# Kernel tuning notes

Measured on AMD Instinct MI355X. Metric: run time of the kernel, lower is better.

The kernel has to match this reference:

```python
import jax, jax.numpy as jnp
import numpy as np

D_MODEL = 1024
N_HEADS = 16
D_K = D_MODEL // N_HEADS


def setup_inputs() -> dict:
    key = jax.random.key(0)
    ks = jax.random.split(key, 11)
    B, S = 2, 2048
    scale = 0.02
    inp = {
        "q": jax.random.normal(ks[0], (B, S, D_MODEL), jnp.float32),
        "k": jax.random.normal(ks[1], (B, S, D_MODEL), jnp.float32),
        "v": jax.random.normal(ks[2], (B, S, D_MODEL), jnp.float32),
        "w_q": jax.random.normal(ks[3], (D_MODEL, D_MODEL), jnp.float32) * scale,
        "b_q": jnp.zeros((D_MODEL,), jnp.float32),
        "w_k": jax.random.normal(ks[4], (D_MODEL, D_MODEL), jnp.float32) * scale,
        "b_k": jnp.zeros((D_MODEL,), jnp.float32),
        "w_v": jax.random.normal(ks[5], (D_MODEL, D_MODEL), jnp.float32) * scale,
        "b_v": jnp.zeros((D_MODEL,), jnp.float32),
        "w_o": jax.random.normal(ks[6], (D_MODEL, D_MODEL), jnp.float32) * scale,
        "b_o": jnp.zeros((D_MODEL,), jnp.float32),
    }
    return inp


def reference(q, k, v, w_q, b_q, w_k, b_k, w_v, b_v, w_o, b_o):
    B, S, _ = q.shape
    # projections (torch Linear: x @ W.T + b); split into heads -> [B, H, S, d]
    def proj(x, w, b):
        return (x @ w.T + b).reshape(B, S, N_HEADS, D_K).transpose(0, 2, 1, 3)
    qh = proj(q, w_q, b_q)
    kh = proj(k, w_k, b_k)
    vh = proj(v, w_v, b_v)
    scores = jnp.einsum("bhqd,bhkd->bhqk", qh, kh) / jnp.sqrt(
        jnp.asarray(D_K, jnp.float32))
    attn = jax.nn.softmax(scores, axis=-1)  # dropout = identity (eval)
    out = jnp.einsum("bhqk,bhkd->bhqd", attn, vh)
    out = out.transpose(0, 2, 1, 3).reshape(B, S, D_MODEL)
    return out @ w_o.T + b_o
```

## Files before the change

### kernel.cpp

```cpp
#include <hip/hip_runtime.h>

typedef unsigned short u16;
typedef unsigned int u32;
typedef __attribute__((ext_vector_type(4))) unsigned short u16x4;
typedef __attribute__((ext_vector_type(8))) unsigned short u16x8;
typedef __attribute__((ext_vector_type(8))) __bf16 bf16x8;
typedef __attribute__((ext_vector_type(4))) float f32x4;
typedef __attribute__((ext_vector_type(16))) float f32x16;

#define SEQ 2048
#define DMODEL 1024
#define LDP 3072
#define MM (DMODEL * DMODEL)
#define SC 0.18033688f

__device__ __forceinline__ u16 f2bf(float f) {
  unsigned u = __builtin_bit_cast(unsigned, f);
  u = (u + 0x7fffu + ((u >> 16) & 1u)) >> 16;
  return (u16)u;
}

__device__ __forceinline__ u32 cvtpk(float lo, float hi) {
  u32 r;
  asm volatile("v_cvt_pk_bf16_f32 %0, %1, %2" : "=v"(r) : "v"(lo), "v"(hi));
  return r;
}

__device__ __forceinline__ float fexp2(float x) {
#if __has_builtin(__builtin_amdgcn_exp2f)
  return __builtin_amdgcn_exp2f(x);
#else
  return exp2f(x);
#endif
}

__device__ __forceinline__ bf16x8 ldbf8(const u16* p) {
  return __builtin_bit_cast(bf16x8, *(const u16x8*)p);
}
__device__ __forceinline__ bf16x8 ldbf8c(const char* p) {
  return __builtin_bit_cast(bf16x8, *(const u16x8*)p);
}

__device__ __forceinline__ f32x4 mfma16(bf16x8 a, bf16x8 b, f32x4 c) {
  return __builtin_amdgcn_mfma_f32_16x16x32_bf16(a, b, c, 0, 0, 0);
}
__device__ __forceinline__ f32x16 mfma32(bf16x8 a, bf16x8 b, f32x16 c) {
  return __builtin_amdgcn_mfma_f32_32x32x16_bf16(a, b, c, 0, 0, 0);
}

__device__ __forceinline__ void gl16(const void* g, void* l) {
  __builtin_amdgcn_global_load_lds(
      (__attribute__((address_space(1))) void*)(size_t)g,
      (__attribute__((address_space(3))) void*)l, 16, 0, 0);
}

__global__ void cast_all_k(const float* __restrict__ q, const float* __restrict__ k,
                           const float* __restrict__ v, const float* __restrict__ wq,
                           const float* __restrict__ wk, const float* __restrict__ wv,
                           const float* __restrict__ wo, u16* __restrict__ dq,
                           u16* __restrict__ dk, u16* __restrict__ dv,
                           u16* __restrict__ wqkv, u16* __restrict__ wob) {
  int b = blockIdx.x;
  const float* s;
  u16* d;
  if (b < 6144) {
    const int z = b >> 11;
    s = z == 0 ? q : z == 1 ? k : v;
    d = z == 0 ? dq : z == 1 ? dk : dv;
    b &= 2047;
  } else {
    const int z = (b - 6144) >> 9;
    s = z == 0 ? wq : z == 1 ? wk : z == 2 ? wv : wo;
    d = z < 3 ? wqkv + (size_t)z * MM : wob;
    b = (b - 6144) & 511;
  }
  const size_t i = ((size_t)b * blockDim.x + threadIdx.x) * 8;
  const float4 a = *(const float4*)(s + i);
  const float4 c = *(const float4*)(s + i + 4);
  u16x8 o;
  o[0] = f2bf(a.x); o[1] = f2bf(a.y); o[2] = f2bf(a.z); o[3] = f2bf(a.w);
  o[4] = f2bf(c.x); o[5] = f2bf(c.y); o[6] = f2bf(c.z); o[7] = f2bf(c.w);
  *(u16x8*)(d + i) = o;
}

template <int OMODE>
__device__ __forceinline__ void gemm_bt_body(const u16* __restrict__ A,
                                             const u16* __restrict__ Bw,
                                             const float* __restrict__ bias,
                                             void* __restrict__ Cv, const int K,
                                             const int ldc, const int ncol0,
                                             const int m0, const int n0,
                                             const float osc) {
  __shared__ u16 As[128 * 32];
  __shared__ u16 Bs[128 * 32];
  const int tid = threadIdx.x;
  const int lane = tid & 63;
  const int w = tid >> 6;
  const int l15 = lane & 15;
  const int lg = lane >> 4;

  f32x4 acc[4][4] = {};

  const int arow = (w >> 1) * 64 + l15;
  const int brow = (w & 1) * 64 + l15;
  const int kfb = lg * 16;

  const int strow = w * 32 + (lane >> 2);
  const u16* Ag = A + (size_t)(m0 + strow) * K + (lane & 3) * 8;
  const u16* Bg = Bw + (size_t)(n0 + strow) * K + (lane & 3) * 8;
  const size_t rstep = (size_t)16 * K;
  char* AsL0 = (char*)As + w * 32 * 64;
  char* AsL1 = AsL0 + 16 * 64;
  char* BsL0 = (char*)Bs + w * 32 * 64;
  char* BsL1 = BsL0 + 16 * 64;

  for (int k0 = 0; k0 < K; k0 += 32) {
    __syncthreads();
    gl16(Ag + k0, AsL0);
    gl16(Ag + k0 + rstep, AsL1);
    gl16(Bg + k0, BsL0);
    gl16(Bg + k0 + rstep, BsL1);
    __syncthreads();
    bf16x8 af[4], bfv[4];
#pragma unroll
    for (int t = 0; t < 4; ++t) {
      af[t] = ldbf8c((char*)As + (arow + t * 16) * 64 + kfb);
      bfv[t] = ldbf8c((char*)Bs + (brow + t * 16) * 64 + kfb);
    }
    __builtin_amdgcn_s_setprio(1);
#pragma unroll
    for (int i = 0; i < 4; ++i)
#pragma unroll
      for (int j = 0; j < 4; ++j) acc[i][j] = mfma16(af[i], bfv[j], acc[i][j]);
    __builtin_amdgcn_s_setprio(0);
  }

  const int mrow = (w >> 1) * 64 + lg * 4;
  const int ncol = (w & 1) * 64 + l15;
#pragma unroll
  for (int j = 0; j < 4; ++j) {
    const int gn = n0 + ncol + j * 16;
    const float bia = bias[gn];
#pragma unroll
    for (int i = 0; i < 4; ++i) {
      const int gmb = m0 + mrow + i * 16;
#pragma unroll
      for (int r = 0; r < 4; ++r) {
        const float val = (acc[i][j][r] + bia) * osc;
        const int gm = gmb + r;
        if (OMODE == 0) {
          ((float*)Cv)[(size_t)gm * ldc + gn] = val;
        } else if (OMODE == 1) {
          ((u16*)Cv)[(size_t)gm * ldc + ncol0 + gn] = f2bf(val);
        } else {
          const int bb = gm >> 11, ss = gm & 2047;
          const int hh = gn >> 6, dd = gn & 63;
          ((u16*)Cv)[(((size_t)(bb * 16 + hh) * 64 + dd) << 11) + ss] = f2bf(val);
        }
      }
    }
  }
}

__global__ __launch_bounds__(256, 3) void gemm_qkv_k(
    const u16* __restrict__ qb, const u16* __restrict__ kb,
    const u16* __restrict__ vb, const u16* __restrict__ wqkv,
    const float* __restrict__ bq, const float* __restrict__ bk,
    const float* __restrict__ bv, u16* __restrict__ proj, u16* __restrict__ vtb) {
  const int b = blockIdx.x;
  const int xcd = b & 7;
  const int i = b >> 3;
  const int z = i >> 5;
  const int j = i & 31;
  const int m0 = (xcd * 4 + (j >> 3)) * 128;
  const int n0 = (j & 7) * 128;
  if (z == 2)
    gemm_bt_body<2>(vb, wqkv + 2 * (size_t)MM, bv, vtb, DMODEL, 0, 0, m0, n0,
                    1.0f);
  else
    gemm_bt_body<1>(z == 0 ? qb : kb, wqkv + (size_t)z * MM, z == 0 ? bq : bk,
                    proj, DMODEL, LDP, z * DMODEL, m0, n0, z == 0 ? SC : 1.0f);
}

__global__ __launch_bounds__(256, 3) void gemm_o_k(const u16* __restrict__ attnb,
                                                   const u16* __restrict__ wob,
                                                   const float* __restrict__ bo,
                                                   float* __restrict__ out) {
  const int b = blockIdx.x;
  const int xcd = b & 7;
  const int i = b >> 3;
  const int m0 = (xcd * 4 + (i >> 3)) * 128;
  const int n0 = (i & 7) * 128;
  gemm_bt_body<0>(attnb, wob, bo, out, DMODEL, DMODEL, 0, m0, n0, 1.0f);
}

__global__ __launch_bounds__(512, 2) void attn_k(const u16* __restrict__ proj,
                                                 const u16* __restrict__ vtb,
                                                 u16* __restrict__ outa) {
  __shared__ __align__(16) char smem[65536];
  const int b = blockIdx.x;
  const int slot = b >> 3;
  const int bh = (b & 7) * 4 + (slot >> 3);
  const int qB = (slot & 7) * 256;
  const int tid = threadIdx.x;
  const int lane = tid & 63;
  const int w = tid >> 6;
  const int g = w >> 2;
  const int wg = w & 3;
  const int tg = tid & 255;
  const size_t rb = (size_t)(bh >> 4) * SEQ;
  const int h = bh & 15;
  const int l31 = lane & 31;
  const int hi = lane >> 5;
  const int swzk = (l31 & 7) << 4;
  const int swzv = (l31 & 15) << 3;

  char* const ksb = smem + g * 32768;
  char* const vsb = ksb + 16384;

  const int qW = qB + wg * 64;
  const u16* qpA = proj + (rb + qW + l31) * LDP + h * 64 + hi * 8;
  const u16* qpB = qpA + (size_t)32 * LDP;
  bf16x8 qfA[4], qfB[4];
#pragma unroll
  for (int km = 0; km < 4; ++km) {
    qfA[km] = ldbf8(qpA + km * 16);
    qfB[km] = ldbf8(qpB + km * 16);
  }

  const int srow = tg >> 2;
  const int scol = (tg & 3) * 32;
  const int scel = scol >> 1;
  const int kz0 = srow * 128 + (scol ^ ((srow & 7) << 4));
  const int kz1 = srow * 128 + ((scol + 16) ^ ((srow & 7) << 4));
  const int vz0 = srow * 128 + (scol ^ ((srow & 15) << 3));
  const int vz1 = srow * 128 + ((scol + 8) ^ ((srow & 15) << 3));
  const int vz2 = srow * 128 + ((scol + 16) ^ ((srow & 15) << 3));
  const int vz3 = srow * 128 + ((scol + 24) ^ ((srow & 15) << 3));
  const u16* kg = proj + rb * LDP + DMODEL + h * 64;
  const u16* vg = vtb + (size_t)bh * 64 * SEQ;
  const int kvbase = g * (SEQ / 2);

  u16x8 ka0, ka1, va0, va1;
  {
    const u16* kr = kg + (size_t)(kvbase + srow) * LDP + scel;
    ka0 = *(const u16x8*)kr;
    ka1 = *(const u16x8*)(kr + 8);
    const u16* vr = vg + (size_t)srow * SEQ + kvbase + scel;
    va0 = *(const u16x8*)vr;
    va1 = *(const u16x8*)(vr + 8);
  }

  f32x16 oaA0 = {}, oaA1 = {}, oaB0 = {}, oaB1 = {};
  float lrunA = 0.f, lrunB = 0.f;
  int p = 0;

  for (int it = 0; it < SEQ / 128; ++it) {
    {
      char* kd = ksb + p * 8192;
      char* vd = vsb + p * 8192;
      *(u16x8*)(kd + kz0) = ka0;
      *(u16x8*)(kd + kz1) = ka1;
      *(u16x4*)(vd + vz0) = *(u16x4*)&va0;
      *(u16x4*)(vd + vz1) = *((u16x4*)&va0 + 1);
      *(u16x4*)(vd + vz2) = *(u16x4*)&va1;
      *(u16x4*)(vd + vz3) = *((u16x4*)&va1 + 1);
    }
    __syncthreads();
    if (it + 1 < SEQ / 128) {
      const int kvn = kvbase + (it + 1) * 64;
      const u16* kr = kg + (size_t)(kvn + srow) * LDP + scel;
      ka0 = *(const u16x8*)kr;
      ka1 = *(const u16x8*)(kr + 8);
      const u16* vr = vg + (size_t)srow * SEQ + kvn + scel;
      va0 = *(const u16x8*)vr;
      va1 = *(const u16x8*)(vr + 8);
    }
    const char* kp = ksb + p * 8192;
    const char* vp = vsb + p * 8192;
    f32x16 sA0 = {}, sA1 = {}, sB0 = {}, sB1 = {};
    __builtin_amdgcn_s_setprio(1);
#pragma unroll
    for (int km = 0; km < 4; ++km) {
      const int co = (km * 32 + hi * 16) ^ swzk;
      const bf16x8 k0 = ldbf8c(kp + l31 * 128 + co);
      const bf16x8 k1 = ldbf8c(kp + (32 + l31) * 128 + co);
      sA0 = mfma32(k0, qfA[km], sA0);
      sB0 = mfma32(k0, qfB[km], sB0);
      sA1 = mfma32(k1, qfA[km], sA1);
      sB1 = mfma32(k1, qfB[km], sB1);
    }
    __builtin_amdgcn_s_setprio(0);

#pragma unroll
    for (int r = 0; r < 16; ++r) sA0[r] = fexp2(sA0[r]);
#pragma unroll
    for (int r = 0; r < 16; ++r) sA1[r] = fexp2(sA1[r]);
#pragma unroll
    for (int r = 0; r < 16; ++r) sB0[r] = fexp2(sB0[r]);
#pragma unroll
    for (int r = 0; r < 16; ++r) sB1[r] = fexp2(sB1[r]);
#define SUM16(V)                                                        \
    ((((V[0] + V[1]) + (V[2] + V[3])) + ((V[4] + V[5]) + (V[6] + V[7]))) + \
     (((V[8] + V[9]) + (V[10] + V[11])) + ((V[12] + V[13]) + (V[14] + V[15]))))
    float rsA = SUM16(sA0) + SUM16(sA1);
    float rsB = SUM16(sB0) + SUM16(sB1);
#undef SUM16
    rsA += __shfl_xor(rsA, 32);
    rsB += __shfl_xor(rsB, 32);
    lrunA += rsA;
    lrunB += rsB;

    __builtin_amdgcn_s_setprio(1);
#define PCHUNK2(SA, SB, G, CB)                                           \
    {                                                                    \
      u16x8 pbuA, pbuB;                                                  \
      ((u32*)&pbuA)[0] = cvtpk(SA[G + 0], SA[G + 1]);                    \
      ((u32*)&pbuA)[1] = cvtpk(SA[G + 2], SA[G + 3]);                    \
      ((u32*)&pbuA)[2] = cvtpk(SA[G + 4], SA[G + 5]);                    \
      ((u32*)&pbuA)[3] = cvtpk(SA[G + 6], SA[G + 7]);                    \
      ((u32*)&pbuB)[0] = cvtpk(SB[G + 0], SB[G + 1]);                    \
      ((u32*)&pbuB)[1] = cvtpk(SB[G + 2], SB[G + 3]);                    \
      ((u32*)&pbuB)[2] = cvtpk(SB[G + 4], SB[G + 5]);                    \
      ((u32*)&pbuB)[3] = cvtpk(SB[G + 6], SB[G + 7]);                    \
      const bf16x8 pbA = __builtin_bit_cast(bf16x8, pbuA);               \
      const bf16x8 pbB = __builtin_bit_cast(bf16x8, pbuB);               \
      const int vc0 = ((CB) + 8 * hi) ^ swzv;                            \
      const int vc1 = ((CB) + 16 + 8 * hi) ^ swzv;                       \
      const char* vr0 = vp + l31 * 128;                                  \
      const char* vr1 = vp + (32 + l31) * 128;                           \
      u16x8 vf0, vf1;                                                    \
      *(u16x4*)&vf0       = *(const u16x4*)(vr0 + vc0);                  \
      *((u16x4*)&vf0 + 1) = *(const u16x4*)(vr0 + vc1);                  \
      *(u16x4*)&vf1       = *(const u16x4*)(vr1 + vc0);                  \
      *((u16x4*)&vf1 + 1) = *(const u16x4*)(vr1 + vc1);                  \
      const bf16x8 v0 = __builtin_bit_cast(bf16x8, vf0);                 \
      const bf16x8 v1 = __builtin_bit_cast(bf16x8, vf1);                 \
      oaA0 = mfma32(v0, pbA, oaA0);                                      \
      oaB0 = mfma32(v0, pbB, oaB0);                                      \
      oaA1 = mfma32(v1, pbA, oaA1);                                      \
      oaB1 = mfma32(v1, pbB, oaB1);                                      \
    }
    PCHUNK2(sA0, sB0, 0, 0)
    PCHUNK2(sA0, sB0, 8, 32)
    PCHUNK2(sA1, sB1, 0, 64)
    PCHUNK2(sA1, sB1, 8, 96)
#undef PCHUNK2
    __builtin_amdgcn_s_setprio(0);
    p ^= 1;
  }

  float* sc = (float*)smem;
  const int col = wg * 64 + lane;
  __syncthreads();
  if (g == 1) {
#pragma unroll
    for (int r = 0; r < 16; ++r) sc[r * 256 + col] = oaA0[r];
#pragma unroll
    for (int r = 0; r < 16; ++r) sc[(16 + r) * 256 + col] = oaA1[r];
    sc[32 * 256 + col] = lrunA;
  }
  __syncthreads();
  if (g == 0) {
#pragma unroll
    for (int r = 0; r < 16; ++r) oaA0[r] += sc[r * 256 + col];
#pragma unroll
    for (int r = 0; r < 16; ++r) oaA1[r] += sc[(16 + r) * 256 + col];
    lrunA += sc[32 * 256 + col];
  }
  __syncthreads();
  if (g == 1) {
#pragma unroll
    for (int r = 0; r < 16; ++r) sc[r * 256 + col] = oaB0[r];
#pragma unroll
    for (int r = 0; r < 16; ++r) sc[(16 + r) * 256 + col] = oaB1[r];
    sc[32 * 256 + col] = lrunB;
  }
  __syncthreads();
  if (g == 0) {
#pragma unroll
    for (int r = 0; r < 16; ++r) oaB0[r] += sc[r * 256 + col];
#pragma unroll
    for (int r = 0; r < 16; ++r) oaB1[r] += sc[(16 + r) * 256 + col];
    lrunB += sc[32 * 256 + col];

    const float invA = 1.0f / lrunA;
    u16* orowA = outa + (rb + qW + l31) * DMODEL + h * 64 + hi * 4;
#pragma unroll
    for (int gg = 0; gg < 4; ++gg) {
      u16x4 st0, st1;
      ((u32*)&st0)[0] = cvtpk(oaA0[4 * gg + 0] * invA, oaA0[4 * gg + 1] * invA);
      ((u32*)&st0)[1] = cvtpk(oaA0[4 * gg + 2] * invA, oaA0[4 * gg + 3] * invA);
      *(u16x4*)(orowA + 8 * gg) = st0;
      ((u32*)&st1)[0] = cvtpk(oaA1[4 * gg + 0] * invA, oaA1[4 * gg + 1] * invA);
      ((u32*)&st1)[1] = cvtpk(oaA1[4 * gg + 2] * invA, oaA1[4 * gg + 3] * invA);
      *(u16x4*)(orowA + 32 + 8 * gg) = st1;
    }
    const float invB = 1.0f / lrunB;
    u16* orowB = orowA + (size_t)32 * DMODEL;
#pragma unroll
    for (int gg = 0; gg < 4; ++gg) {
      u16x4 st0, st1;
      ((u32*)&st0)[0] = cvtpk(oaB0[4 * gg + 0] * invB, oaB0[4 * gg + 1] * invB);
      ((u32*)&st0)[1] = cvtpk(oaB0[4 * gg + 2] * invB, oaB0[4 * gg + 3] * invB);
      *(u16x4*)(orowB + 8 * gg) = st0;
      ((u32*)&st1)[0] = cvtpk(oaB1[4 * gg + 0] * invB, oaB1[4 * gg + 1] * invB);
      ((u32*)&st1)[1] = cvtpk(oaB1[4 * gg + 2] * invB, oaB1[4 * gg + 3] * invB);
      *(u16x4*)(orowB + 32 + 8 * gg) = st1;
    }
  }
}

extern "C" void kernel_launch(void* const* d_in, const int* in_sizes, int n_in,
                              void* d_out, int out_size, void* d_ws, size_t ws_size,
                              hipStream_t stream) {
  const float* q  = (const float*)d_in[0];
  const float* k  = (const float*)d_in[1];
  const float* v  = (const float*)d_in[2];
  const float* wq = (const float*)d_in[3];
  const float* bq = (const float*)d_in[4];
  const float* wk = (const float*)d_in[5];
  const float* bk = (const float*)d_in[6];
  const float* wv = (const float*)d_in[7];
  const float* bv = (const float*)d_in[8];
  const float* wo = (const float*)d_in[9];
  const float* bo = (const float*)d_in[10];

  const size_t NTOK = (size_t)2 * SEQ;
  const size_t NELE = NTOK * DMODEL;
  u16* qb    = (u16*)d_ws;
  u16* kb    = qb + NELE;
  u16* vb    = kb + NELE;
  u16* wqkv  = vb + NELE;
  u16* wob   = wqkv + 3 * (size_t)MM;
  u16* projb = wob + (size_t)MM;
  u16* vtb   = projb + NTOK * LDP;
  u16* attnb = qb;

  cast_all_k<<<8192, 256, 0, stream>>>(q, k, v, wq, wk, wv, wo, qb, kb, vb,
                                       wqkv, wob);
  gemm_qkv_k<<<768, 256, 0, stream>>>(qb, kb, vb, wqkv, bq, bk, bv, projb, vtb);
  attn_k<<<256, 512, 0, stream>>>(projb, vtb, attnb);
  gemm_o_k<<<256, 256, 0, stream>>>(attnb, wob, bo, (float*)d_out);
}
```

Baseline: 118.1 us.

## Stage K/V tiles via direct global-to-LDS loads with permuted V layout

Replaces the register-staged K/V loads (global to registers, then swizzled LDS stores) with direct global-to-LDS 16-byte loads (gl16) into a double buffer, issued one iteration ahead. To make this work, the V projection epilogue writes V^T with a permuted sequence index, so the V tile in LDS can be read with single 16-byte ldbf8c reads instead of paired 8-byte reads. This removes the VGPR round trip and the LDS store instructions, and it moves the barrier to the end of each iteration. The cost is a dependence on the producer-side permutation and a changed synchronisation pattern that must still order the async LDS writes correctly.

```diff
diff --git a/kernel.cpp b/kernel.cpp
--- a/kernel.cpp
+++ b/kernel.cpp
@@ -154,8 +154,9 @@
           ((u16*)Cv)[(size_t)gm * ldc + ncol0 + gn] = f2bf(val);
         } else {
           const int bb = gm >> 11, ss = gm & 2047;
+          const int ssp = (ss & ~12) | ((ss & 4) << 1) | ((ss & 8) >> 1);
           const int hh = gn >> 6, dd = gn & 63;
-          ((u16*)Cv)[(((size_t)(bb * 16 + hh) * 64 + dd) << 11) + ss] = f2bf(val);
+          ((u16*)Cv)[(((size_t)(bb * 16 + hh) * 64 + dd) << 11) + ssp] = f2bf(val);
         }
       }
     }
@@ -207,16 +208,13 @@
   const int w = tid >> 6;
   const int g = w >> 2;
   const int wg = w & 3;
-  const int tg = tid & 255;
   const size_t rb = (size_t)(bh >> 4) * SEQ;
   const int h = bh & 15;
   const int l31 = lane & 31;
   const int hi = lane >> 5;
   const int swzk = (l31 & 7) << 4;
-  const int swzv = (l31 & 15) << 3;
-
-  char* const ksb = smem + g * 32768;
-  char* const vsb = ksb + 16384;
+
+  char* const gbase = smem + g * 32768;
 
   const int qW = qB + wg * 64;
   const u16* qpA = proj + (rb + qW + l31) * LDP + h * 64 + hi * 8;
@@ -228,56 +226,38 @@
     qfB[km] = ldbf8(qpB + km * 16);
   }
 
-  const int srow = tg >> 2;
-  const int scol = (tg & 3) * 32;
-  const int scel = scol >> 1;
-  const int kz0 = srow * 128 + (scol ^ ((srow & 7) << 4));
-  const int kz1 = srow * 128 + ((scol + 16) ^ ((srow & 7) << 4));
-  const int vz0 = srow * 128 + (scol ^ ((srow & 15) << 3));
-  const int vz1 = srow * 128 + ((scol + 8) ^ ((srow & 15) << 3));
-  const int vz2 = srow * 128 + ((scol + 16) ^ ((srow & 15) << 3));
-  const int vz3 = srow * 128 + ((scol + 24) ^ ((srow & 15) << 3));
+  const int cxe = ((lane & 7) ^ (lane >> 3)) * 8;
+  const int row0 = wg * 16 + (lane >> 3);
+  const int row1 = row0 + 8;
   const u16* kg = proj + rb * LDP + DMODEL + h * 64;
   const u16* vg = vtb + (size_t)bh * 64 * SEQ;
   const int kvbase = g * (SEQ / 2);
-
-  u16x8 ka0, ka1, va0, va1;
-  {
-    const u16* kr = kg + (size_t)(kvbase + srow) * LDP + scel;
-    ka0 = *(const u16x8*)kr;
-    ka1 = *(const u16x8*)(kr + 8);
-    const u16* vr = vg + (size_t)srow * SEQ + kvbase + scel;
-    va0 = *(const u16x8*)vr;
-    va1 = *(const u16x8*)(vr + 8);
+  const u16* ks0 = kg + (size_t)(kvbase + row0) * LDP + cxe;
+  const u16* ks1 = kg + (size_t)(kvbase + row1) * LDP + cxe;
+  const u16* vs0 = vg + (size_t)row0 * SEQ + kvbase + cxe;
+  const u16* vs1 = vg + (size_t)row1 * SEQ + kvbase + cxe;
+
+#define STAGE(P, KOFF)                                                   \
+  {                                                                      \
+    char* kb_ = gbase + (P) * 8192;                                      \
+    char* vb_ = gbase + 16384 + (P) * 8192;                              \
+    gl16(ks0 + (size_t)(KOFF) * LDP, kb_ + (wg * 2 + 0) * 1024);         \
+    gl16(ks1 + (size_t)(KOFF) * LDP, kb_ + (wg * 2 + 1) * 1024);         \
+    gl16(vs0 + (KOFF), vb_ + (wg * 2 + 0) * 1024);                       \
+    gl16(vs1 + (KOFF), vb_ + (wg * 2 + 1) * 1024);                       \
   }
 
   f32x16 oaA0 = {}, oaA1 = {}, oaB0 = {}, oaB1 = {};
   float lrunA = 0.f, lrunB = 0.f;
   int p = 0;
 
+  STAGE(0, 0);
+  __syncthreads();
+
   for (int it = 0; it < SEQ / 128; ++it) {
-    {
-      char* kd = ksb + p * 8192;
-      char* vd = vsb + p * 8192;
-      *(u16x8*)(kd + kz0) = ka0;
-      *(u16x8*)(kd + kz1) = ka1;
-      *(u16x4*)(vd + vz0) = *(u16x4*)&va0;
-      *(u16x4*)(vd + vz1) = *((u16x4*)&va0 + 1);
-      *(u16x4*)(vd + vz2) = *(u16x4*)&va1;
-      *(u16x4*)(vd + vz3) = *((u16x4*)&va1 + 1);
-    }
-    __syncthreads();
-    if (it + 1 < SEQ / 128) {
-      const int kvn = kvbase + (it + 1) * 64;
-      const u16* kr = kg + (size_t)(kvn + srow) * LDP + scel;
-      ka0 = *(const u16x8*)kr;
-      ka1 = *(const u16x8*)(kr + 8);
-      const u16* vr = vg + (size_t)srow * SEQ + kvn + scel;
-      va0 = *(const u16x8*)vr;
-      va1 = *(const u16x8*)(vr + 8);
-    }
-    const char* kp = ksb + p * 8192;
-    const char* vp = vsb + p * 8192;
+    if (it + 1 < SEQ / 128) STAGE(p ^ 1, (it + 1) * 64);
+    const char* kp = gbase + p * 8192;
+    const char* vp = gbase + 16384 + p * 8192;
     f32x16 sA0 = {}, sA1 = {}, sB0 = {}, sB1 = {};
     __builtin_amdgcn_s_setprio(1);
 #pragma unroll
@@ -312,7 +292,7 @@
     lrunB += rsB;
 
     __builtin_amdgcn_s_setprio(1);
-#define PCHUNK2(SA, SB, G, CB)                                           \
+#define PCHUNK2(SA, SB, G, M)                                            \
     {                                                                    \
       u16x8 pbuA, pbuB;                                                  \
       ((u32*)&pbuA)[0] = cvtpk(SA[G + 0], SA[G + 1]);                    \
@@ -325,34 +305,27 @@
       ((u32*)&pbuB)[3] = cvtpk(SB[G + 6], SB[G + 7]);                    \
       const bf16x8 pbA = __builtin_bit_cast(bf16x8, pbuA);               \
       const bf16x8 pbB = __builtin_bit_cast(bf16x8, pbuB);               \
-      const int vc0 = ((CB) + 8 * hi) ^ swzv;                            \
-      const int vc1 = ((CB) + 16 + 8 * hi) ^ swzv;                       \
-      const char* vr0 = vp + l31 * 128;                                  \
-      const char* vr1 = vp + (32 + l31) * 128;                           \
-      u16x8 vf0, vf1;                                                    \
-      *(u16x4*)&vf0       = *(const u16x4*)(vr0 + vc0);                  \
-      *((u16x4*)&vf0 + 1) = *(const u16x4*)(vr0 + vc1);                  \
-      *(u16x4*)&vf1       = *(const u16x4*)(vr1 + vc0);                  \
-      *((u16x4*)&vf1 + 1) = *(const u16x4*)(vr1 + vc1);                  \
-      const bf16x8 v0 = __builtin_bit_cast(bf16x8, vf0);                 \
-      const bf16x8 v1 = __builtin_bit_cast(bf16x8, vf1);                 \
+      const int vc = ((M) * 32 + hi * 16) ^ swzk;                        \
+      const bf16x8 v0 = ldbf8c(vp + l31 * 128 + vc);                     \
+      const bf16x8 v1 = ldbf8c(vp + (32 + l31) * 128 + vc);              \
       oaA0 = mfma32(v0, pbA, oaA0);                                      \
       oaB0 = mfma32(v0, pbB, oaB0);                                      \
       oaA1 = mfma32(v1, pbA, oaA1);                                      \
       oaB1 = mfma32(v1, pbB, oaB1);                                      \
     }
     PCHUNK2(sA0, sB0, 0, 0)
-    PCHUNK2(sA0, sB0, 8, 32)
-    PCHUNK2(sA1, sB1, 0, 64)
-    PCHUNK2(sA1, sB1, 8, 96)
+    PCHUNK2(sA0, sB0, 8, 1)
+    PCHUNK2(sA1, sB1, 0, 2)
+    PCHUNK2(sA1, sB1, 8, 3)
 #undef PCHUNK2
     __builtin_amdgcn_s_setprio(0);
+    __syncthreads();
     p ^= 1;
   }
+#undef STAGE
 
   float* sc = (float*)smem;
   const int col = wg * 64 + lane;
-  __syncthreads();
   if (g == 1) {
 #pragma unroll
     for (int r = 0; r < 16; ++r) sc[r * 256 + col] = oaA0[r];
```

Measured after the change: 120.2 us. Within noise of the previous version (+1.8%).
